# Performance work log

Measured on AMD Instinct MI355X. Metric: run time of the kernel, lower is better.

The kernel has to match this reference:

```python
import jax, jax.numpy as jnp
import numpy as np

EPS = 1e-07
N = 524288      # samples (columns x layers)
C = 42          # n_channel
NC = 8          # n_constituent
HID = [5, 4, 4] # hidden widths per MLP
OUT = 3         # absorbed / transmitted / reflected split


def _make_mlp_params(key, n_in):
    """Stacked per-channel MLP params: weights [C,out,in], biases [C,out]."""
    dims = [n_in] + HID + [OUT]
    Ws, bs = [], []
    for i in range(len(dims) - 1):
        key, kw, kb = jax.random.split(key, 3)
        W = jax.random.uniform(kw, (C, dims[i + 1], dims[i]), minval=-1.0, maxval=1.0)
        if i < len(dims) - 2:  # hidden bias ~ U(0.9, 1.1)
            b = jax.random.uniform(kb, (C, dims[i + 1]), minval=0.9, maxval=1.1)
        else:                  # output bias ~ U(-0.1, 0.1)
            b = jax.random.uniform(kb, (C, dims[i + 1]), minval=-0.1, maxval=0.1)
        Ws.append(W)
        bs.append(b)
    return Ws, bs


def setup_inputs() -> dict:
    key = jax.random.key(0)
    k0, k1, k2, k3, kd, kf = jax.random.split(key, 6)
    inp = {
        "tau": jax.random.uniform(k0, (N, C, NC), dtype=jnp.float32) * 0.5,
        "mu_direct": jax.random.uniform(k1, (N, 1), minval=0.05, maxval=1.0, dtype=jnp.float32),
        "mu_diffuse": jax.random.uniform(k2, (N, 1), minval=0.05, maxval=1.0, dtype=jnp.float32),
        "constituents": jax.random.uniform(k3, (N, NC), dtype=jnp.float32),
    }
    Wd, bd = _make_mlp_params(kd, NC + 1)  # direct nets take mu appended
    Wf, bf = _make_mlp_params(kf, NC)      # diffuse nets
    for i in range(4):
        inp[f"Wd{i}"], inp[f"bd{i}"] = Wd[i], bd[i]
        inp[f"Wf{i}"], inp[f"bf{i}"] = Wf[i], bf[i]
    return inp


def _batched_mlp_softmax(x, Ws, bs):
    # x: [N, n_in] shared across channels; Ws[i]: [C, out, in]; bs[i]: [C, out]
    h = jnp.einsum('ni,coi->nco', x, Ws[0]) + bs[0]
    h = jax.nn.relu(h)
    for W, b in zip(Ws[1:-1], bs[1:-1]):
        h = jax.nn.relu(jnp.einsum('nci,coi->nco', h, W) + b)
    logits = jnp.einsum('nci,coi->nco', h, Ws[-1]) + bs[-1]  # [N, C, 3]
    return jax.nn.softmax(logits, axis=-1)


def reference(tau, mu_direct, mu_diffuse, constituents,
              Wd0, bd0, Wd1, bd1, Wd2, bd2, Wd3, bd3,
              Wf0, bf0, Wf1, bf1, Wf2, bf2, Wf3, bf3):
    tau_total = jnp.sum(tau, axis=2)                    # [N, C]
    t_direct = jnp.exp(-tau_total / (mu_direct + EPS))  # mu [N,1] broadcasts over C
    t_diffuse = jnp.exp(-tau_total / (mu_diffuse + EPS))

    cons_direct = jnp.concatenate(
        [constituents / (mu_direct + EPS), mu_direct], axis=1)  # [N, NC+1]

    e_split_direct = _batched_mlp_softmax(
        cons_direct, [Wd0, Wd1, Wd2, Wd3], [bd0, bd1, bd2, bd3])   # [N, C, 3]
    e_split_diffuse = _batched_mlp_softmax(
        constituents, [Wf0, Wf1, Wf2, Wf3], [bf0, bf1, bf2, bf3])  # [N, C, 3]

    return (t_direct, t_diffuse, e_split_direct, e_split_diffuse)
```

## Files before the change

kernel.cpp:

```cpp
#include <hip/hip_runtime.h>

#define EPS 1e-7f
#define CCH 42
#define NCON 8

typedef float v4f __attribute__((ext_vector_type(4)));
typedef float v2f __attribute__((ext_vector_type(2)));

template<int NIN>
__device__ __forceinline__ void mlp_softmax3(
    const float x[NIN], int c,
    const float* __restrict__ W0, const float* __restrict__ b0,
    const float* __restrict__ W1, const float* __restrict__ b1,
    const float* __restrict__ W2, const float* __restrict__ b2,
    const float* __restrict__ W3, const float* __restrict__ b3,
    float o[3])
{
    float h0[5];
#pragma unroll
    for (int j = 0; j < 5; ++j) {
        const float* w = W0 + (c * 5 + j) * NIN;
        float a = b0[c * 5 + j];
#pragma unroll
        for (int i = 0; i < NIN; ++i) a = fmaf(x[i], w[i], a);
        h0[j] = fmaxf(a, 0.0f);
    }
    float h1[4];
#pragma unroll
    for (int j = 0; j < 4; ++j) {
        const float* w = W1 + (c * 4 + j) * 5;
        float a = b1[c * 4 + j];
#pragma unroll
        for (int i = 0; i < 5; ++i) a = fmaf(h0[i], w[i], a);
        h1[j] = fmaxf(a, 0.0f);
    }
    float h2[4];
#pragma unroll
    for (int j = 0; j < 4; ++j) {
        const float* w = W2 + (c * 4 + j) * 4;
        float a = b2[c * 4 + j];
#pragma unroll
        for (int i = 0; i < 4; ++i) a = fmaf(h1[i], w[i], a);
        h2[j] = fmaxf(a, 0.0f);
    }
    float lg[3];
#pragma unroll
    for (int j = 0; j < 3; ++j) {
        const float* w = W3 + (c * 3 + j) * 4;
        float a = b3[c * 3 + j];
#pragma unroll
        for (int i = 0; i < 4; ++i) a = fmaf(h2[i], w[i], a);
        lg[j] = a;
    }
    float m = fmaxf(fmaxf(lg[0], lg[1]), lg[2]);
    float e0 = __expf(lg[0] - m);
    float e1 = __expf(lg[1] - m);
    float e2 = __expf(lg[2] - m);
    float r = __fdividef(1.0f, e0 + e1 + e2);
    o[0] = e0 * r;
    o[1] = e1 * r;
    o[2] = e2 * r;
}

__global__ __launch_bounds__(384, 6) void k_fused(
    const float* __restrict__ tau,
    const float* __restrict__ mu_direct,
    const float* __restrict__ mu_diffuse,
    const float* __restrict__ cons,
    const float* __restrict__ Wd0, const float* __restrict__ bd0,
    const float* __restrict__ Wf0, const float* __restrict__ bf0,
    const float* __restrict__ Wd1, const float* __restrict__ bd1,
    const float* __restrict__ Wf1, const float* __restrict__ bf1,
    const float* __restrict__ Wd2, const float* __restrict__ bd2,
    const float* __restrict__ Wf2, const float* __restrict__ bf2,
    const float* __restrict__ Wd3, const float* __restrict__ bd3,
    const float* __restrict__ Wf3, const float* __restrict__ bf3,
    float* __restrict__ out, int N)
{
    __shared__ float es[64 * 127];
    const int tid  = threadIdx.x;
    const int lane = tid & 63;
    const int wave = tid >> 6;
    const int n0   = blockIdx.x * 64;
    const int n    = n0 + lane;
    const bool direct = (blockIdx.y == 0);
    const size_t nctot = (size_t)N * CCH;

    float4 c0 = *(const float4*)(cons + (size_t)n * NCON);
    float4 c1 = *(const float4*)(cons + (size_t)n * NCON + 4);
    float mu  = direct ? mu_direct[n] : 0.0f;
    __builtin_amdgcn_sched_barrier(0);

    const int nblk = gridDim.x * 2;
    const int cid  = blockIdx.y * gridDim.x + blockIdx.x;
    const int per  = (int)(nctot / nblk);
    const int base_e = cid * per;
    v4f ta[4], tb[4];
#pragma unroll
    for (int it = 0; it < 4; ++it) {
        int off = it * 384 + tid;
        if (off < per) {
            const v4f* t4 = (const v4f*)tau + ((size_t)base_e + off) * 2;
            ta[it] = __builtin_nontemporal_load(t4);
            tb[it] = __builtin_nontemporal_load(t4 + 1);
        }
    }
    __builtin_amdgcn_sched_barrier(0);

    float x[9] = {c0.x, c0.y, c0.z, c0.w, c1.x, c1.y, c1.z, c1.w, 0.0f};
    if (direct) {
        float inv = __fdividef(1.0f, mu + EPS);
#pragma unroll
        for (int i = 0; i < 8; ++i) x[i] *= inv;
        x[8] = mu;
#pragma unroll 1
        for (int ci = 0; ci < 7; ++ci) {
            int c = __builtin_amdgcn_readfirstlane(wave * 7 + ci);
            float o[3];
            mlp_softmax3<9>(x, c, Wd0, bd0, Wd1, bd1, Wd2, bd2, Wd3, bd3, o);
#pragma unroll
            for (int k = 0; k < 3; ++k) es[lane * 127 + c * 3 + k] = o[k];
        }
    } else {
#pragma unroll 1
        for (int ci = 0; ci < 7; ++ci) {
            int c = __builtin_amdgcn_readfirstlane(wave * 7 + ci);
            float o[3];
            mlp_softmax3<8>(x, c, Wf0, bf0, Wf1, bf1, Wf2, bf2, Wf3, bf3, o);
#pragma unroll
            for (int k = 0; k < 3; ++k) es[lane * 127 + c * 3 + k] = o[k];
        }
    }
    __syncthreads();

    float* base = out + (direct ? 2 : 5) * nctot + (size_t)n0 * (CCH * 3);
    for (int idx = tid; idx < 64 * 63; idx += 384) {
        int r = idx / 63;
        int q = idx - r * 63;
        v2f v;
        v.x = es[r * 127 + 2 * q];
        v.y = es[r * 127 + 2 * q + 1];
        __builtin_nontemporal_store(v, (v2f*)base + idx);
    }

#pragma unroll
    for (int it = 0; it < 4; ++it) {
        int off = it * 384 + tid;
        if (off < per) {
            int e = base_e + off;
            v4f a = ta[it];
            v4f b = tb[it];
            float s = ((a.x + a.y) + (a.z + a.w)) + ((b.x + b.y) + (b.z + b.w));
            int nn = e / CCH;
            float md = mu_direct[nn] + EPS;
            float mf = mu_diffuse[nn] + EPS;
            __builtin_nontemporal_store(__expf(__fdividef(-s, md)), out + e);
            __builtin_nontemporal_store(__expf(__fdividef(-s, mf)), out + nctot + e);
        }
    }
}

extern "C" void kernel_launch(void* const* d_in, const int* in_sizes, int n_in,
                              void* d_out, int out_size, void* d_ws, size_t ws_size,
                              hipStream_t stream) {
    const float* tau  = (const float*)d_in[0];
    const float* mud  = (const float*)d_in[1];
    const float* muf  = (const float*)d_in[2];
    const float* cons = (const float*)d_in[3];
    const float* Wd0 = (const float*)d_in[4];  const float* bd0 = (const float*)d_in[5];
    const float* Wf0 = (const float*)d_in[6];  const float* bf0 = (const float*)d_in[7];
    const float* Wd1 = (const float*)d_in[8];  const float* bd1 = (const float*)d_in[9];
    const float* Wf1 = (const float*)d_in[10]; const float* bf1 = (const float*)d_in[11];
    const float* Wd2 = (const float*)d_in[12]; const float* bd2 = (const float*)d_in[13];
    const float* Wf2 = (const float*)d_in[14]; const float* bf2 = (const float*)d_in[15];
    const float* Wd3 = (const float*)d_in[16]; const float* bd3 = (const float*)d_in[17];
    const float* Wf3 = (const float*)d_in[18]; const float* bf3 = (const float*)d_in[19];
    float* out = (float*)d_out;

    int N = in_sizes[1];
    dim3 grid(N / 64, 2);
    k_fused<<<grid, 384, 0, stream>>>(tau, mud, muf, cons,
                                      Wd0, bd0, Wf0, bf0,
                                      Wd1, bd1, Wf1, bf1,
                                      Wd2, bd2, Wf2, bf2,
                                      Wd3, bd3, Wf3, bf3,
                                      out, N);
}
```

Measured before the change: 294.9 us.

## Interleave transmittance stores with MLP loop, prefetch mu, widen split stores

Moves the tau-sum/exp transmittance writes into the per-channel MLP loop so their global stores overlap with MLP compute rather than following the block barrier. The mu_direct/mu_diffuse values for those elements are loaded up front with the other prefetches, and the partition is reworked so each block handles half of its own 64 samples' tau range. The shared staging buffer drops its padding to 126 floats per row and is 16-byte aligned, so the split output can be written with 128-bit stores instead of 64-bit ones. The cost is possible LDS bank conflicts from the unpadded stride, and more registers held live across the loop.

```diff
diff --git a/kernel.cpp b/kernel.cpp
--- a/kernel.cpp
+++ b/kernel.cpp
@@ -5,7 +5,6 @@
 #define NCON 8
 
 typedef float v4f __attribute__((ext_vector_type(4)));
-typedef float v2f __attribute__((ext_vector_type(2)));
 
 template<int NIN>
 __device__ __forceinline__ void mlp_softmax3(
@@ -77,7 +76,7 @@
     const float* __restrict__ Wf3, const float* __restrict__ bf3,
     float* __restrict__ out, int N)
 {
-    __shared__ float es[64 * 127];
+    __shared__ __align__(16) float es[64 * 126];
     const int tid  = threadIdx.x;
     const int lane = tid & 63;
     const int wave = tid >> 6;
@@ -86,15 +85,24 @@
     const bool direct = (blockIdx.y == 0);
     const size_t nctot = (size_t)N * CCH;
 
+    const int per    = 32 * CCH;
+    const int base_e = blockIdx.x * (64 * CCH) + (direct ? 0 : per);
+
     float4 c0 = *(const float4*)(cons + (size_t)n * NCON);
     float4 c1 = *(const float4*)(cons + (size_t)n * NCON + 4);
     float mu  = direct ? mu_direct[n] : 0.0f;
+    float mdv[4], mfv[4];
+#pragma unroll
+    for (int it = 0; it < 4; ++it) {
+        int off = it * 384 + tid;
+        if (off < per) {
+            int nn = (base_e + off) / CCH;
+            mdv[it] = mu_direct[nn];
+            mfv[it] = mu_diffuse[nn];
+        }
+    }
     __builtin_amdgcn_sched_barrier(0);
 
-    const int nblk = gridDim.x * 2;
-    const int cid  = blockIdx.y * gridDim.x + blockIdx.x;
-    const int per  = (int)(nctot / nblk);
-    const int base_e = cid * per;
     v4f ta[4], tb[4];
 #pragma unroll
     for (int it = 0; it < 4; ++it) {
@@ -113,49 +121,42 @@
 #pragma unroll
         for (int i = 0; i < 8; ++i) x[i] *= inv;
         x[8] = mu;
+    }
 #pragma unroll 1
-        for (int ci = 0; ci < 7; ++ci) {
-            int c = __builtin_amdgcn_readfirstlane(wave * 7 + ci);
-            float o[3];
+    for (int ci = 0; ci < 7; ++ci) {
+        int c = __builtin_amdgcn_readfirstlane(wave * 7 + ci);
+        float o[3];
+        if (direct)
             mlp_softmax3<9>(x, c, Wd0, bd0, Wd1, bd1, Wd2, bd2, Wd3, bd3, o);
-#pragma unroll
-            for (int k = 0; k < 3; ++k) es[lane * 127 + c * 3 + k] = o[k];
-        }
-    } else {
-#pragma unroll 1
-        for (int ci = 0; ci < 7; ++ci) {
-            int c = __builtin_amdgcn_readfirstlane(wave * 7 + ci);
-            float o[3];
+        else
             mlp_softmax3<8>(x, c, Wf0, bf0, Wf1, bf1, Wf2, bf2, Wf3, bf3, o);
 #pragma unroll
-            for (int k = 0; k < 3; ++k) es[lane * 127 + c * 3 + k] = o[k];
+        for (int k = 0; k < 3; ++k) es[lane * 126 + c * 3 + k] = o[k];
+
+        if (ci >= 2 && ci <= 5) {
+            int it = ci - 2;
+            int off = it * 384 + tid;
+            if (off < per) {
+                int e = base_e + off;
+                v4f a = ta[it & 3];
+                v4f b = tb[it & 3];
+                float s = ((a.x + a.y) + (a.z + a.w)) + ((b.x + b.y) + (b.z + b.w));
+                float md = mdv[it & 3] + EPS;
+                float mf = mfv[it & 3] + EPS;
+                __builtin_nontemporal_store(__expf(__fdividef(-s, md)), out + e);
+                __builtin_nontemporal_store(__expf(__fdividef(-s, mf)), out + nctot + e);
+            }
         }
     }
     __syncthreads();
 
     float* base = out + (direct ? 2 : 5) * nctot + (size_t)n0 * (CCH * 3);
-    for (int idx = tid; idx < 64 * 63; idx += 384) {
-        int r = idx / 63;
-        int q = idx - r * 63;
-        v2f v;
-        v.x = es[r * 127 + 2 * q];
-        v.y = es[r * 127 + 2 * q + 1];
-        __builtin_nontemporal_store(v, (v2f*)base + idx);
-    }
-
 #pragma unroll
-    for (int it = 0; it < 4; ++it) {
-        int off = it * 384 + tid;
-        if (off < per) {
-            int e = base_e + off;
-            v4f a = ta[it];
-            v4f b = tb[it];
-            float s = ((a.x + a.y) + (a.z + a.w)) + ((b.x + b.y) + (b.z + b.w));
-            int nn = e / CCH;
-            float md = mu_direct[nn] + EPS;
-            float mf = mu_diffuse[nn] + EPS;
-            __builtin_nontemporal_store(__expf(__fdividef(-s, md)), out + e);
-            __builtin_nontemporal_store(__expf(__fdividef(-s, mf)), out + nctot + e);
+    for (int iter = 0; iter < 6; ++iter) {
+        int idx = iter * 384 + tid;
+        if (idx < 2016) {
+            v4f v = ((const v4f*)es)[idx];
+            __builtin_nontemporal_store(v, (v4f*)base + idx);
         }
     }
 }
```

Result: slower. 370.9 us (+25.8%).

## Interleave transmittance exp stores with per-channel MLP compute and prefetch mu values

Applied to the files above, without the earlier changes.

Moves the tau-sum/exp transmittance work out of the kernel tail and interleaves it in four batches between the per-channel MLP evaluations. Its global stores can then overlap with ALU-heavy MLP work instead of queuing behind the final LDS-to-global softmax write. The mu_direct/mu_diffuse lookups are hoisted to the kernel start so their latency hides behind the tau loads. The element partition is now fixed at 32*42 per block, assuming each block's tau slice matches its own 64 samples. This also makes the two y-blocks of one x-block cover adjacent halves.

```diff
diff --git a/kernel.cpp b/kernel.cpp
--- a/kernel.cpp
+++ b/kernel.cpp
@@ -60,6 +60,24 @@
     o[0] = e0 * r;
     o[1] = e1 * r;
     o[2] = e2 * r;
+}
+
+template<int IT>
+__device__ __forceinline__ void phase_c_batch(
+    const v4f ta[4], const v4f tb[4], const float mdv[4], const float mfv[4],
+    float* __restrict__ out, size_t nctot, int base_e, int per, int tid)
+{
+    int off = IT * 384 + tid;
+    if (off < per) {
+        int e = base_e + off;
+        v4f a = ta[IT];
+        v4f b = tb[IT];
+        float s = ((a.x + a.y) + (a.z + a.w)) + ((b.x + b.y) + (b.z + b.w));
+        float md = mdv[IT] + EPS;
+        float mf = mfv[IT] + EPS;
+        __builtin_nontemporal_store(__expf(__fdividef(-s, md)), out + e);
+        __builtin_nontemporal_store(__expf(__fdividef(-s, mf)), out + nctot + e);
+    }
 }
 
 __global__ __launch_bounds__(384, 6) void k_fused(
@@ -86,15 +104,24 @@
     const bool direct = (blockIdx.y == 0);
     const size_t nctot = (size_t)N * CCH;
 
+    const int per    = 32 * CCH;
+    const int base_e = blockIdx.x * (64 * CCH) + (direct ? 0 : per);
+
     float4 c0 = *(const float4*)(cons + (size_t)n * NCON);
     float4 c1 = *(const float4*)(cons + (size_t)n * NCON + 4);
     float mu  = direct ? mu_direct[n] : 0.0f;
-    __builtin_amdgcn_sched_barrier(0);
-
-    const int nblk = gridDim.x * 2;
-    const int cid  = blockIdx.y * gridDim.x + blockIdx.x;
-    const int per  = (int)(nctot / nblk);
-    const int base_e = cid * per;
+    float mdv[4], mfv[4];
+#pragma unroll
+    for (int it = 0; it < 4; ++it) {
+        int off = it * 384 + tid;
+        if (off < per) {
+            int nn = (base_e + off) / CCH;
+            mdv[it] = mu_direct[nn];
+            mfv[it] = mu_diffuse[nn];
+        }
+    }
+    __builtin_amdgcn_sched_barrier(0);
+
     v4f ta[4], tb[4];
 #pragma unroll
     for (int it = 0; it < 4; ++it) {
@@ -113,24 +140,33 @@
 #pragma unroll
         for (int i = 0; i < 8; ++i) x[i] *= inv;
         x[8] = mu;
-#pragma unroll 1
-        for (int ci = 0; ci < 7; ++ci) {
-            int c = __builtin_amdgcn_readfirstlane(wave * 7 + ci);
-            float o[3];
+    }
+    auto do_ch = [&](int ci) {
+        int c = __builtin_amdgcn_readfirstlane(wave * 7 + ci);
+        float o[3];
+        if (direct)
             mlp_softmax3<9>(x, c, Wd0, bd0, Wd1, bd1, Wd2, bd2, Wd3, bd3, o);
-#pragma unroll
-            for (int k = 0; k < 3; ++k) es[lane * 127 + c * 3 + k] = o[k];
-        }
-    } else {
-#pragma unroll 1
-        for (int ci = 0; ci < 7; ++ci) {
-            int c = __builtin_amdgcn_readfirstlane(wave * 7 + ci);
-            float o[3];
+        else
             mlp_softmax3<8>(x, c, Wf0, bf0, Wf1, bf1, Wf2, bf2, Wf3, bf3, o);
 #pragma unroll
-            for (int k = 0; k < 3; ++k) es[lane * 127 + c * 3 + k] = o[k];
-        }
-    }
+        for (int k = 0; k < 3; ++k) es[lane * 127 + c * 3 + k] = o[k];
+    };
+
+    do_ch(0);
+    do_ch(1);
+    do_ch(2);
+    phase_c_batch<0>(ta, tb, mdv, mfv, out, nctot, base_e, per, tid);
+    __builtin_amdgcn_sched_barrier(0);
+    do_ch(3);
+    phase_c_batch<1>(ta, tb, mdv, mfv, out, nctot, base_e, per, tid);
+    __builtin_amdgcn_sched_barrier(0);
+    do_ch(4);
+    phase_c_batch<2>(ta, tb, mdv, mfv, out, nctot, base_e, per, tid);
+    __builtin_amdgcn_sched_barrier(0);
+    do_ch(5);
+    phase_c_batch<3>(ta, tb, mdv, mfv, out, nctot, base_e, per, tid);
+    __builtin_amdgcn_sched_barrier(0);
+    do_ch(6);
     __syncthreads();
 
     float* base = out + (direct ? 2 : 5) * nctot + (size_t)n0 * (CCH * 3);
@@ -141,22 +177,6 @@
         v.x = es[r * 127 + 2 * q];
         v.y = es[r * 127 + 2 * q + 1];
         __builtin_nontemporal_store(v, (v2f*)base + idx);
-    }
-
-#pragma unroll
-    for (int it = 0; it < 4; ++it) {
-        int off = it * 384 + tid;
-        if (off < per) {
-            int e = base_e + off;
-            v4f a = ta[it];
-            v4f b = tb[it];
-            float s = ((a.x + a.y) + (a.z + a.w)) + ((b.x + b.y) + (b.z + b.w));
-            int nn = e / CCH;
-            float md = mu_direct[nn] + EPS;
-            float mf = mu_diffuse[nn] + EPS;
-            __builtin_nontemporal_store(__expf(__fdividef(-s, md)), out + e);
-            __builtin_nontemporal_store(__expf(__fdividef(-s, mf)), out + nctot + e);
-        }
     }
 }
 
```

Result: no change. 296.9 us (+0.7%).

## Split tau loads into two phases, shuffle mu values, and compact LDS staging

Applied to the files above, without the earlier changes.

Each block now covers the tau rows of its own 32 samples, so the mu values come from wavefront shuffles instead of per-element global gathers. Half of the tau loads and transmission stores are issued before the MLP work finishes and the rest after, which lowers register pressure and lets the occupancy hint rise from 6 to 8. The LDS staging buffer loses its padding row so the split output is copied out as contiguous vec2 reads in a fixed unrolled loop. The risks are LDS bank conflicts from dropping the padding and reliance on N being a multiple of 64.

```diff
diff --git a/kernel.cpp b/kernel.cpp
--- a/kernel.cpp
+++ b/kernel.cpp
@@ -62,7 +62,7 @@
     o[2] = e2 * r;
 }
 
-__global__ __launch_bounds__(384, 6) void k_fused(
+__global__ __launch_bounds__(384, 8) void k_fused(
     const float* __restrict__ tau,
     const float* __restrict__ mu_direct,
     const float* __restrict__ mu_diffuse,
@@ -77,7 +77,7 @@
     const float* __restrict__ Wf3, const float* __restrict__ bf3,
     float* __restrict__ out, int N)
 {
-    __shared__ float es[64 * 127];
+    __shared__ __align__(16) float es[64 * 126];
     const int tid  = threadIdx.x;
     const int lane = tid & 63;
     const int wave = tid >> 6;
@@ -86,40 +86,38 @@
     const bool direct = (blockIdx.y == 0);
     const size_t nctot = (size_t)N * CCH;
 
+    const int per        = 32 * CCH;
+    const int base_local = direct ? 0 : per;
+    const int base_e     = n0 * CCH + base_local;
+
     float4 c0 = *(const float4*)(cons + (size_t)n * NCON);
     float4 c1 = *(const float4*)(cons + (size_t)n * NCON + 4);
-    float mu  = direct ? mu_direct[n] : 0.0f;
+    float mud_own = mu_direct[n];
+    float muf_own = mu_diffuse[n];
     __builtin_amdgcn_sched_barrier(0);
 
-    const int nblk = gridDim.x * 2;
-    const int cid  = blockIdx.y * gridDim.x + blockIdx.x;
-    const int per  = (int)(nctot / nblk);
-    const int base_e = cid * per;
-    v4f ta[4], tb[4];
-#pragma unroll
-    for (int it = 0; it < 4; ++it) {
-        int off = it * 384 + tid;
-        if (off < per) {
-            const v4f* t4 = (const v4f*)tau + ((size_t)base_e + off) * 2;
-            ta[it] = __builtin_nontemporal_load(t4);
-            tb[it] = __builtin_nontemporal_load(t4 + 1);
-        }
+    v4f ta0, tb0, ta1, tb1;
+    {
+        const v4f* t4 = (const v4f*)tau + ((size_t)base_e + tid) * 2;
+        ta0 = t4[0]; tb0 = t4[1];
+        const v4f* t5 = (const v4f*)tau + ((size_t)base_e + 384 + tid) * 2;
+        ta1 = t5[0]; tb1 = t5[1];
     }
     __builtin_amdgcn_sched_barrier(0);
 
     float x[9] = {c0.x, c0.y, c0.z, c0.w, c1.x, c1.y, c1.z, c1.w, 0.0f};
     if (direct) {
-        float inv = __fdividef(1.0f, mu + EPS);
+        float inv = __fdividef(1.0f, mud_own + EPS);
 #pragma unroll
         for (int i = 0; i < 8; ++i) x[i] *= inv;
-        x[8] = mu;
+        x[8] = mud_own;
 #pragma unroll 1
         for (int ci = 0; ci < 7; ++ci) {
             int c = __builtin_amdgcn_readfirstlane(wave * 7 + ci);
             float o[3];
             mlp_softmax3<9>(x, c, Wd0, bd0, Wd1, bd1, Wd2, bd2, Wd3, bd3, o);
 #pragma unroll
-            for (int k = 0; k < 3; ++k) es[lane * 127 + c * 3 + k] = o[k];
+            for (int k = 0; k < 3; ++k) es[lane * 126 + c * 3 + k] = o[k];
         }
     } else {
 #pragma unroll 1
@@ -128,35 +126,75 @@
             float o[3];
             mlp_softmax3<8>(x, c, Wf0, bf0, Wf1, bf1, Wf2, bf2, Wf3, bf3, o);
 #pragma unroll
-            for (int k = 0; k < 3; ++k) es[lane * 127 + c * 3 + k] = o[k];
-        }
-    }
+            for (int k = 0; k < 3; ++k) es[lane * 126 + c * 3 + k] = o[k];
+        }
+    }
+
+    {
+        int off = tid;
+        float s = ((ta0.x + ta0.y) + (ta0.z + ta0.w)) + ((tb0.x + tb0.y) + (tb0.z + tb0.w));
+        int nnl = (base_local + off) / CCH;
+        float md = __shfl(mud_own, nnl) + EPS;
+        float mf = __shfl(muf_own, nnl) + EPS;
+        int e = base_e + off;
+        __builtin_nontemporal_store(__expf(__fdividef(-s, md)), out + e);
+        __builtin_nontemporal_store(__expf(__fdividef(-s, mf)), out + nctot + e);
+    }
+    {
+        int off = 384 + tid;
+        float s = ((ta1.x + ta1.y) + (ta1.z + ta1.w)) + ((tb1.x + tb1.y) + (tb1.z + tb1.w));
+        int nnl = (base_local + off) / CCH;
+        float md = __shfl(mud_own, nnl) + EPS;
+        float mf = __shfl(muf_own, nnl) + EPS;
+        int e = base_e + off;
+        __builtin_nontemporal_store(__expf(__fdividef(-s, md)), out + e);
+        __builtin_nontemporal_store(__expf(__fdividef(-s, mf)), out + nctot + e);
+    }
+
+    v4f ta2, tb2, ta3, tb3;
+    const bool b3act = (3 * 384 + tid) < per;
+    {
+        const v4f* p2 = (const v4f*)tau + ((size_t)base_e + 2 * 384 + tid) * 2;
+        ta2 = p2[0]; tb2 = p2[1];
+        if (b3act) {
+            const v4f* p3 = (const v4f*)tau + ((size_t)base_e + 3 * 384 + tid) * 2;
+            ta3 = p3[0]; tb3 = p3[1];
+        }
+    }
+    __builtin_amdgcn_sched_barrier(0);
     __syncthreads();
 
-    float* base = out + (direct ? 2 : 5) * nctot + (size_t)n0 * (CCH * 3);
-    for (int idx = tid; idx < 64 * 63; idx += 384) {
-        int r = idx / 63;
-        int q = idx - r * 63;
-        v2f v;
-        v.x = es[r * 127 + 2 * q];
-        v.y = es[r * 127 + 2 * q + 1];
-        __builtin_nontemporal_store(v, (v2f*)base + idx);
-    }
-
-#pragma unroll
-    for (int it = 0; it < 4; ++it) {
-        int off = it * 384 + tid;
-        if (off < per) {
-            int e = base_e + off;
-            v4f a = ta[it];
-            v4f b = tb[it];
-            float s = ((a.x + a.y) + (a.z + a.w)) + ((b.x + b.y) + (b.z + b.w));
-            int nn = e / CCH;
-            float md = mu_direct[nn] + EPS;
-            float mf = mu_diffuse[nn] + EPS;
-            __builtin_nontemporal_store(__expf(__fdividef(-s, md)), out + e);
-            __builtin_nontemporal_store(__expf(__fdividef(-s, mf)), out + nctot + e);
-        }
+    {
+        float* base = out + (direct ? 2 : 5) * nctot + (size_t)n0 * (CCH * 3);
+#pragma unroll
+        for (int k = 0; k < 11; ++k) {
+            int idx = k * 384 + tid;
+            if (idx < 4032) {
+                v2f v = ((const v2f*)es)[idx];
+                __builtin_nontemporal_store(v, (v2f*)base + idx);
+            }
+        }
+    }
+
+    {
+        int off = 2 * 384 + tid;
+        float s = ((ta2.x + ta2.y) + (ta2.z + ta2.w)) + ((tb2.x + tb2.y) + (tb2.z + tb2.w));
+        int nnl = (base_local + off) / CCH;
+        float md = __shfl(mud_own, nnl) + EPS;
+        float mf = __shfl(muf_own, nnl) + EPS;
+        int e = base_e + off;
+        __builtin_nontemporal_store(__expf(__fdividef(-s, md)), out + e);
+        __builtin_nontemporal_store(__expf(__fdividef(-s, mf)), out + nctot + e);
+    }
+    if (b3act) {
+        int off = 3 * 384 + tid;
+        float s = ((ta3.x + ta3.y) + (ta3.z + ta3.w)) + ((tb3.x + tb3.y) + (tb3.z + tb3.w));
+        int nnl = (base_local + off) / CCH;
+        float md = __shfl(mud_own, nnl) + EPS;
+        float mf = __shfl(muf_own, nnl) + EPS;
+        int e = base_e + off;
+        __builtin_nontemporal_store(__expf(__fdividef(-s, md)), out + e);
+        __builtin_nontemporal_store(__expf(__fdividef(-s, mf)), out + nctot + e);
     }
 }
 
```

After: 284.0 us (median of 2 runs). -3.7%, faster.
